# Optimization experiments

Measured on AMD Instinct MI355X. Metric: run time of the kernel, lower is better.

Reference implementation:

```python
import jax, jax.numpy as jnp
import numpy as np

N, D = 8192, 1024


def setup_inputs() -> dict:
    key = jax.random.key(0)
    k1, k2 = jax.random.split(key)
    x = jax.random.normal(k1, (N, D), dtype=jnp.float32)
    # scale weight like a trained linear layer (~1/sqrt(D)) so softmax isn't fully saturated
    W = jax.random.normal(k2, (D, D), dtype=jnp.float32) * (1.0 / np.sqrt(D))
    b = jnp.zeros((D,), dtype=jnp.float32)
    recency_weight = jnp.full((1,), -0.5, dtype=jnp.float32)  # nn.Parameter init in source
    return {"x": x, "W": W, "b": b, "recency_weight": recency_weight}


def reference(x, W, b, recency_weight):
    # linear + relu
    x_proj = jax.nn.relu(x @ W.T + b)          # [N, D]
    # tied self-matmul
    scores = x_proj @ x_proj.T                  # [N, N]
    n = x.shape[0]
    idx = jnp.arange(n)
    # causal mask: upper triangle strictly above diagonal (use_current_timestep=True)
    upper = idx[None, :] > idx[:, None]         # [N, N] bool
    scores = jnp.where(upper, -jnp.inf, scores)
    # recency bias: toeplitz |i - j|, zeroed on masked (upper) part, scaled by recency_weight
    dist = jnp.abs(idx[:, None] - idx[None, :]).astype(scores.dtype)
    recency = recency_weight[0] * jnp.where(upper, 0.0, dist)
    scores = scores + recency
    return jax.nn.softmax(scores, axis=1)       # [N, N] lower-triangular attention
```

## Files before the change

kernel.cpp:

```cpp
#include <hip/hip_runtime.h>
#include <math.h>

#define NR 8192
#define DIM 1024

typedef __attribute__((ext_vector_type(8))) short bf16x8;
typedef __attribute__((ext_vector_type(4))) float f32x4;

static __device__ __forceinline__ unsigned short f2bf(float f) {
  unsigned int u = __float_as_uint(f);
  u += 0x7fffu + ((u >> 16) & 1u);
  return (unsigned short)(u >> 16);
}

static __device__ __forceinline__ float bf2f(unsigned short u) {
  return __uint_as_float(((unsigned int)u) << 16);
}

static __device__ __forceinline__ void gload_lds16(const void* g, void* lds) {
  __builtin_amdgcn_global_load_lds(
      (const __attribute__((address_space(1))) unsigned int*)g,
      (__attribute__((address_space(3))) unsigned int*)lds, 16, 0, 0);
}

__global__ __launch_bounds__(256) void cvt_bf16(const float* __restrict__ in,
                                                unsigned short* __restrict__ outp,
                                                int n4) {
  int i = blockIdx.x * 256 + threadIdx.x;
  if (i < n4) {
    float4 v = ((const float4*)in)[i];
    ushort4 o;
    o.x = f2bf(v.x); o.y = f2bf(v.y); o.z = f2bf(v.z); o.w = f2bf(v.w);
    ((ushort4*)outp)[i] = o;
  }
}

static __device__ __forceinline__ void gemm_core(const unsigned short* A,
                                                 const unsigned short* B,
                                                 int m0, int n0, int K,
                                                 short* As, short* Bs,
                                                 f32x4 acc[4][4]) {
  const int tid  = threadIdx.x;
  const int lane = tid & 63;
  const int wave = tid >> 6;
  const int wr = wave >> 1, wc = wave & 1;
  const int ch_r = lane >> 2;
  const int ch_c = (lane & 3) * 8;

  for (int kt = 0; kt < K; kt += 32) {
#pragma unroll
    for (int c = 0; c < 4; ++c) {
      int ch = wave * 4 + c;
      if (ch < 8) {
        const unsigned short* g = A + (size_t)(m0 + ch * 16 + ch_r) * DIM + kt + ch_c;
        gload_lds16(g, As + ch * 512);
      } else {
        const unsigned short* g = B + (size_t)(n0 + (ch - 8) * 16 + ch_r) * DIM + kt + ch_c;
        gload_lds16(g, Bs + (ch - 8) * 512);
      }
    }
    asm volatile("s_waitcnt vmcnt(0)" ::: "memory");
    __syncthreads();

    bf16x8 af[4], bfr[4];
#pragma unroll
    for (int m = 0; m < 4; ++m)
      af[m] = *(const bf16x8*)(As + (wr * 64 + m * 16 + (lane & 15)) * 32 + (lane >> 4) * 8);
#pragma unroll
    for (int n = 0; n < 4; ++n)
      bfr[n] = *(const bf16x8*)(Bs + (wc * 64 + n * 16 + (lane & 15)) * 32 + (lane >> 4) * 8);
#pragma unroll
    for (int m = 0; m < 4; ++m)
#pragma unroll
      for (int n = 0; n < 4; ++n)
        acc[m][n] = __builtin_amdgcn_mfma_f32_16x16x32_bf16(af[m], bfr[n], acc[m][n], 0, 0, 0);
    __syncthreads();
  }
}

__global__ __launch_bounds__(256) void gemm1_relu(const unsigned short* __restrict__ Xb,
                                                  const unsigned short* __restrict__ Wb,
                                                  const float* __restrict__ bias,
                                                  unsigned short* __restrict__ XP) {
  __shared__ short As[4096], Bs[4096];
  const int m0 = blockIdx.y * 128, n0 = blockIdx.x * 128;
  f32x4 acc[4][4] = {};
  gemm_core(Xb, Wb, m0, n0, DIM, As, Bs, acc);

  const int lane = threadIdx.x & 63, wave = threadIdx.x >> 6;
  const int wr = wave >> 1, wc = wave & 1, g = lane >> 4, li = lane & 15;
#pragma unroll
  for (int m = 0; m < 4; ++m)
#pragma unroll
    for (int n = 0; n < 4; ++n) {
      int col = n0 + wc * 64 + n * 16 + li;
      float bv = bias[col];
#pragma unroll
      for (int r = 0; r < 4; ++r) {
        int row = m0 + wr * 64 + m * 16 + g * 4 + r;
        float v = fmaxf(acc[m][n][r] + bv, 0.0f);
        XP[(size_t)row * DIM + col] = f2bf(v);
      }
    }
}

__global__ __launch_bounds__(256) void gemm2_scores(const unsigned short* __restrict__ XP,
                                                    const float* __restrict__ rwp,
                                                    unsigned short* __restrict__ Pb,
                                                    float* __restrict__ wsm,
                                                    float* __restrict__ wsl) {
  int t = ((int)blockIdx.x & 7) * 260 + ((int)blockIdx.x >> 3);
  int by = (int)((sqrtf(8.0f * (float)t + 1.0f) - 1.0f) * 0.5f);
  while ((by + 1) * (by + 2) / 2 <= t) ++by;
  while (by * (by + 1) / 2 > t) --by;
  const int bx = t - by * (by + 1) / 2;

  __shared__ short As[4096], Bs[4096];
  const int m0 = by * 128, n0 = bx * 128;
  f32x4 acc[4][4] = {};
  gemm_core(XP, XP, m0, n0, DIM, As, Bs, acc);

  const float rw = rwp[0];
  const int lane = threadIdx.x & 63, wave = threadIdx.x >> 6;
  const int wr = wave >> 1, wc = wave & 1, g = lane >> 4, li = lane & 15;
  const int pcol = bx * 2 + wc;

#pragma unroll
  for (int m = 0; m < 4; ++m) {
#pragma unroll
    for (int r = 0; r < 4; ++r) {
      const int row = m0 + wr * 64 + m * 16 + g * 4 + r;
      float s[4];
      float mx = -INFINITY;
#pragma unroll
      for (int n = 0; n < 4; ++n) {
        int col = n0 + wc * 64 + n * 16 + li;
        float v = acc[m][n][r];
        v = (col <= row) ? v + rw * (float)(row - col) : -INFINITY;
        s[n] = v;
        mx = fmaxf(mx, v);
      }
#pragma unroll
      for (int off = 1; off < 16; off <<= 1) mx = fmaxf(mx, __shfl_xor(mx, off));
      float se = 0.0f;
#pragma unroll
      for (int n = 0; n < 4; ++n) {
        float e = __expf(s[n] - mx);
        se += e;
        int col = n0 + wc * 64 + n * 16 + li;
        if (col <= row) Pb[(size_t)row * NR + col] = f2bf(e);
      }
#pragma unroll
      for (int off = 1; off < 16; off <<= 1) se += __shfl_xor(se, off);
      if (li == 0) {
        wsm[(size_t)row * 128 + pcol] = mx;
        wsl[(size_t)row * 128 + pcol] = se;
      }
    }
  }
}

__global__ __launch_bounds__(256) void rowstats(const float* __restrict__ wsm,
                                                const float* __restrict__ wsl,
                                                float* __restrict__ Ms,
                                                float* __restrict__ Ls) {
  const int row = blockIdx.x * 4 + (threadIdx.x >> 6);
  const int lane = threadIdx.x & 63;
  const int nch = (row >> 6) + 1;
  float m0v = (lane < nch) ? wsm[(size_t)row * 128 + lane] : -INFINITY;
  float m1v = (lane + 64 < nch) ? wsm[(size_t)row * 128 + lane + 64] : -INFINITY;
  float mx = fmaxf(m0v, m1v);
#pragma unroll
  for (int off = 1; off < 64; off <<= 1) mx = fmaxf(mx, __shfl_xor(mx, off));
  float l = 0.0f;
  if (lane < nch)      l += wsl[(size_t)row * 128 + lane]      * __expf(m0v - mx);
  if (lane + 64 < nch) l += wsl[(size_t)row * 128 + lane + 64] * __expf(m1v - mx);
#pragma unroll
  for (int off = 1; off < 64; off <<= 1) l += __shfl_xor(l, off);
  if (lane == 0) { Ms[row] = mx; Ls[row] = 1.0f / l; }
}

__global__ __launch_bounds__(256) void normk(const unsigned short* __restrict__ Pb,
                                             float* __restrict__ out,
                                             const float* __restrict__ Ms,
                                             const float* __restrict__ Ls,
                                             const float* __restrict__ wsm) {
  const size_t idx = (size_t)blockIdx.x * 256 + threadIdx.x;
  const int row = (int)(idx >> 11);
  const int j0 = (int)(idx & 2047) * 4;
  float4* p = (float4*)out + idx;
  if (j0 > row) {
    float4 z; z.x = 0.f; z.y = 0.f; z.z = 0.f; z.w = 0.f;
    *p = z;
    return;
  }
  const float M = Ms[row];
  const float sc = __expf(wsm[(size_t)row * 128 + (j0 >> 6)] - M) * Ls[row];
  ushort4 q = *(const ushort4*)(Pb + (size_t)row * NR + j0);
  float4 o;
  o.x = bf2f(q.x) * sc;
  o.y = bf2f(q.y) * sc;
  o.z = bf2f(q.z) * sc;
  o.w = bf2f(q.w) * sc;
  if (j0 + 3 > row) {
    if (j0 + 1 > row) o.y = 0.f;
    if (j0 + 2 > row) o.z = 0.f;
    o.w = 0.f;
  }
  *p = o;
}

extern "C" void kernel_launch(void* const* d_in, const int* in_sizes, int n_in,
                              void* d_out, int out_size, void* d_ws, size_t ws_size,
                              hipStream_t stream) {
  const float* x  = (const float*)d_in[0];
  const float* W  = (const float*)d_in[1];
  const float* b  = (const float*)d_in[2];
  const float* rw = (const float*)d_in[3];
  float* out = (float*)d_out;

  char* ws = (char*)d_ws;
  unsigned short* Xb = (unsigned short*)(ws);
  unsigned short* Wb = (unsigned short*)(ws + (size_t)(16 << 20));
  unsigned short* XP = (unsigned short*)(ws + (size_t)(18 << 20));
  float* wsm = (float*)(ws + (size_t)(34 << 20));
  float* wsl = (float*)(ws + (size_t)(38 << 20));
  float* Ms  = (float*)(ws + (size_t)(42 << 20));
  float* Ls  = (float*)(ws + (size_t)(42 << 20) + 32768);
  unsigned short* Pb = (unsigned short*)(ws + (size_t)(64 << 20));

  cvt_bf16<<<NR * DIM / 4 / 256, 256, 0, stream>>>(x, Xb, NR * DIM / 4);
  cvt_bf16<<<DIM * DIM / 4 / 256, 256, 0, stream>>>(W, Wb, DIM * DIM / 4);
  gemm1_relu<<<dim3(DIM / 128, NR / 128), 256, 0, stream>>>(Xb, Wb, b, XP);
  gemm2_scores<<<2080, 256, 0, stream>>>(XP, rw, Pb, wsm, wsl);
  rowstats<<<NR / 4, 256, 0, stream>>>(wsm, wsl, Ms, Ls);
  normk<<<(NR / 4) * (NR / 256), 256, 0, stream>>>(Pb, out, Ms, Ls, wsm);
}
```

Before: 453.3 us.

## Use row self-dot as softmax max bound, accumulate row sums atomically

Measured after the change: 460.7 us. No clear change (+1.6%).

```diff
diff --git a/kernel.cpp b/kernel.cpp
--- a/kernel.cpp
+++ b/kernel.cpp
@@ -21,6 +21,11 @@
   __builtin_amdgcn_global_load_lds(
       (const __attribute__((address_space(1))) unsigned int*)g,
       (__attribute__((address_space(3))) unsigned int*)lds, 16, 0, 0);
+}
+
+__global__ __launch_bounds__(256) void zerok(float* __restrict__ p, int n) {
+  int i = blockIdx.x * 256 + threadIdx.x;
+  if (i < n) p[i] = 0.0f;
 }
 
 __global__ __launch_bounds__(256) void cvt_bf16(const float* __restrict__ in,
@@ -81,7 +86,8 @@
 __global__ __launch_bounds__(256) void gemm1_relu(const unsigned short* __restrict__ Xb,
                                                   const unsigned short* __restrict__ Wb,
                                                   const float* __restrict__ bias,
-                                                  unsigned short* __restrict__ XP) {
+                                                  unsigned short* __restrict__ XP,
+                                                  float* __restrict__ diag) {
   __shared__ short As[4096], Bs[4096];
   const int m0 = blockIdx.y * 128, n0 = blockIdx.x * 128;
   f32x4 acc[4][4] = {};
@@ -89,26 +95,34 @@
 
   const int lane = threadIdx.x & 63, wave = threadIdx.x >> 6;
   const int wr = wave >> 1, wc = wave & 1, g = lane >> 4, li = lane & 15;
-#pragma unroll
-  for (int m = 0; m < 4; ++m)
-#pragma unroll
-    for (int n = 0; n < 4; ++n) {
-      int col = n0 + wc * 64 + n * 16 + li;
-      float bv = bias[col];
-#pragma unroll
-      for (int r = 0; r < 4; ++r) {
-        int row = m0 + wr * 64 + m * 16 + g * 4 + r;
-        float v = fmaxf(acc[m][n][r] + bv, 0.0f);
+  float bv[4];
+#pragma unroll
+  for (int n = 0; n < 4; ++n) bv[n] = bias[n0 + wc * 64 + n * 16 + li];
+#pragma unroll
+  for (int m = 0; m < 4; ++m) {
+#pragma unroll
+    for (int r = 0; r < 4; ++r) {
+      int row = m0 + wr * 64 + m * 16 + g * 4 + r;
+      float ds = 0.0f;
+#pragma unroll
+      for (int n = 0; n < 4; ++n) {
+        int col = n0 + wc * 64 + n * 16 + li;
+        float v = fmaxf(acc[m][n][r] + bv[n], 0.0f);
         XP[(size_t)row * DIM + col] = f2bf(v);
+        ds += v * v;
       }
+#pragma unroll
+      for (int off = 1; off < 16; off <<= 1) ds += __shfl_xor(ds, off);
+      if (li == 0) atomicAdd(&diag[row], ds);
     }
+  }
 }
 
 __global__ __launch_bounds__(256) void gemm2_scores(const unsigned short* __restrict__ XP,
                                                     const float* __restrict__ rwp,
                                                     unsigned short* __restrict__ Pb,
-                                                    float* __restrict__ wsm,
-                                                    float* __restrict__ wsl) {
+                                                    const float* __restrict__ diag,
+                                                    float* __restrict__ Lrow) {
   int t = ((int)blockIdx.x & 7) * 260 + ((int)blockIdx.x >> 3);
   int by = (int)((sqrtf(8.0f * (float)t + 1.0f) - 1.0f) * 0.5f);
   while ((by + 1) * (by + 2) / 2 <= t) ++by;
@@ -123,68 +137,33 @@
   const float rw = rwp[0];
   const int lane = threadIdx.x & 63, wave = threadIdx.x >> 6;
   const int wr = wave >> 1, wc = wave & 1, g = lane >> 4, li = lane & 15;
-  const int pcol = bx * 2 + wc;
 
 #pragma unroll
   for (int m = 0; m < 4; ++m) {
 #pragma unroll
     for (int r = 0; r < 4; ++r) {
       const int row = m0 + wr * 64 + m * 16 + g * 4 + r;
-      float s[4];
-      float mx = -INFINITY;
+      const float dg = diag[row];
+      float se = 0.0f;
 #pragma unroll
       for (int n = 0; n < 4; ++n) {
         int col = n0 + wc * 64 + n * 16 + li;
         float v = acc[m][n][r];
         v = (col <= row) ? v + rw * (float)(row - col) : -INFINITY;
-        s[n] = v;
-        mx = fmaxf(mx, v);
-      }
-#pragma unroll
-      for (int off = 1; off < 16; off <<= 1) mx = fmaxf(mx, __shfl_xor(mx, off));
-      float se = 0.0f;
-#pragma unroll
-      for (int n = 0; n < 4; ++n) {
-        float e = __expf(s[n] - mx);
+        float e = __expf(v - dg);
         se += e;
-        int col = n0 + wc * 64 + n * 16 + li;
         if (col <= row) Pb[(size_t)row * NR + col] = f2bf(e);
       }
 #pragma unroll
       for (int off = 1; off < 16; off <<= 1) se += __shfl_xor(se, off);
-      if (li == 0) {
-        wsm[(size_t)row * 128 + pcol] = mx;
-        wsl[(size_t)row * 128 + pcol] = se;
-      }
+      if (li == 0) atomicAdd(&Lrow[row], se);
     }
   }
-}
-
-__global__ __launch_bounds__(256) void rowstats(const float* __restrict__ wsm,
-                                                const float* __restrict__ wsl,
-                                                float* __restrict__ Ms,
-                                                float* __restrict__ Ls) {
-  const int row = blockIdx.x * 4 + (threadIdx.x >> 6);
-  const int lane = threadIdx.x & 63;
-  const int nch = (row >> 6) + 1;
-  float m0v = (lane < nch) ? wsm[(size_t)row * 128 + lane] : -INFINITY;
-  float m1v = (lane + 64 < nch) ? wsm[(size_t)row * 128 + lane + 64] : -INFINITY;
-  float mx = fmaxf(m0v, m1v);
-#pragma unroll
-  for (int off = 1; off < 64; off <<= 1) mx = fmaxf(mx, __shfl_xor(mx, off));
-  float l = 0.0f;
-  if (lane < nch)      l += wsl[(size_t)row * 128 + lane]      * __expf(m0v - mx);
-  if (lane + 64 < nch) l += wsl[(size_t)row * 128 + lane + 64] * __expf(m1v - mx);
-#pragma unroll
-  for (int off = 1; off < 64; off <<= 1) l += __shfl_xor(l, off);
-  if (lane == 0) { Ms[row] = mx; Ls[row] = 1.0f / l; }
 }
 
 __global__ __launch_bounds__(256) void normk(const unsigned short* __restrict__ Pb,
                                              float* __restrict__ out,
-                                             const float* __restrict__ Ms,
-                                             const float* __restrict__ Ls,
-                                             const float* __restrict__ wsm) {
+                                             const float* __restrict__ Lrow) {
   const size_t idx = (size_t)blockIdx.x * 256 + threadIdx.x;
   const int row = (int)(idx >> 11);
   const int j0 = (int)(idx & 2047) * 4;
@@ -194,8 +173,7 @@
     *p = z;
     return;
   }
-  const float M = Ms[row];
-  const float sc = __expf(wsm[(size_t)row * 128 + (j0 >> 6)] - M) * Ls[row];
+  const float sc = __builtin_amdgcn_rcpf(Lrow[row]);
   ushort4 q = *(const ushort4*)(Pb + (size_t)row * NR + j0);
   float4 o;
   o.x = bf2f(q.x) * sc;
@@ -223,16 +201,14 @@
   unsigned short* Xb = (unsigned short*)(ws);
   unsigned short* Wb = (unsigned short*)(ws + (size_t)(16 << 20));
   unsigned short* XP = (unsigned short*)(ws + (size_t)(18 << 20));
-  float* wsm = (float*)(ws + (size_t)(34 << 20));
-  float* wsl = (float*)(ws + (size_t)(38 << 20));
-  float* Ms  = (float*)(ws + (size_t)(42 << 20));
-  float* Ls  = (float*)(ws + (size_t)(42 << 20) + 32768);
+  float* diag = (float*)(ws + (size_t)(34 << 20));
+  float* Lrow = (float*)(ws + (size_t)(34 << 20) + 32768);
   unsigned short* Pb = (unsigned short*)(ws + (size_t)(64 << 20));
 
+  zerok<<<(2 * NR + 255) / 256, 256, 0, stream>>>(diag, 2 * NR);
   cvt_bf16<<<NR * DIM / 4 / 256, 256, 0, stream>>>(x, Xb, NR * DIM / 4);
   cvt_bf16<<<DIM * DIM / 4 / 256, 256, 0, stream>>>(W, Wb, DIM * DIM / 4);
-  gemm1_relu<<<dim3(DIM / 128, NR / 128), 256, 0, stream>>>(Xb, Wb, b, XP);
-  gemm2_scores<<<2080, 256, 0, stream>>>(XP, rw, Pb, wsm, wsl);
-  rowstats<<<NR / 4, 256, 0, stream>>>(wsm, wsl, Ms, Ls);
-  normk<<<(NR / 4) * (NR / 256), 256, 0, stream>>>(Pb, out, Ms, Ls, wsm);
-}
+  gemm1_relu<<<dim3(DIM / 128, NR / 128), 256, 0, stream>>>(Xb, Wb, b, XP, diag);
+  gemm2_scores<<<2080, 256, 0, stream>>>(XP, rw, Pb, diag, Lrow);
+  normk<<<(NR / 4) * (NR / 256), 256, 0, stream>>>(Pb, out, Lrow);
+}
```
